# Optimization experiments

Hardware: AMD Instinct MI355X
Metric: run time of the kernel (lower is better)

## Reference

```python
import jax, jax.numpy as jnp
import numpy as np

B, L, D, H = 4, 2048, 1024, 16
DH = D // H
THETA = 100000.0


def setup_inputs() -> dict:
    key = jax.random.key(0)
    k1, k2, k3 = jax.random.split(key, 3)
    std_w = (2.0 / (D + 3 * D)) ** 0.5
    std_o = (2.0 / (D + D)) ** 0.5
    return {
        "x": jax.random.normal(k1, (B, L, D), dtype=jnp.float32),
        "W": jax.random.normal(k2, (3 * D, D), dtype=jnp.float32) * std_w,
        "Wo": jax.random.normal(k3, (D, D), dtype=jnp.float32) * std_o,
    }


def _rope(t):
    # t: [B, H, L, DH]; interleaved pair rotation as in the torch module
    pos = jnp.arange(L, dtype=jnp.float32)
    inv_freq = 1.0 / THETA ** (jnp.arange(0, DH, 2, dtype=jnp.float32) / DH)
    ang = pos[:, None] * inv_freq[None, :]            # [L, DH/2]
    cos = jnp.cos(ang)[:, :, None]                    # [L, DH/2, 1]
    sin = jnp.sin(ang)[:, :, None]
    tp = t.reshape(*t.shape[:-1], DH // 2, 2)         # pairs (x1, x2)
    x1, x2 = tp[..., 0], tp[..., 1]
    rot = jnp.stack([-x2, x1], axis=-1)               # [-x2, x1]
    out = tp * cos + rot * sin
    return out.reshape(*t.shape)


def reference(x, W, Wo):
    # fused QKV projection: weight layout is (t h d) along output dim
    qkv = jnp.einsum('bld,ed->ble', x, W)             # [B, L, 3D]
    qkv = qkv.reshape(B, L, 3, H, DH)
    qkv = jnp.transpose(qkv, (0, 3, 1, 2, 4))         # [B, H, L, 3, DH]
    Q, K, V = qkv[..., 0, :], qkv[..., 1, :], qkv[..., 2, :]
    Q, K = _rope(Q), _rope(K)
    scores = jnp.einsum('bhqd,bhkd->bhqk', Q, K) / (DH ** 0.5)
    causal = jnp.tril(jnp.ones((L, L), dtype=bool))
    scores = jnp.where(causal, scores, -jnp.inf)
    attn = jax.nn.softmax(scores, axis=-1)
    out = jnp.einsum('bhqk,bhkd->bhqd', attn, V)      # [B, H, L, DH]
    out = jnp.transpose(out, (0, 2, 1, 3)).reshape(B, L, D)
    return jnp.einsum('bld,ed->ble', out, Wo)
```

## Files before the change

kernel.cpp:

```cpp
#include <hip/hip_runtime.h>
#include <cstddef>
#include <cstdint>


typedef unsigned short u16;
typedef short bf16x8 __attribute__((ext_vector_type(8)));
typedef float f32x4 __attribute__((ext_vector_type(4)));

#define B_   4
#define L_   2048
#define H_   16
#define DH_  64
#define D_   1024
#define E3_  3072

__device__ __forceinline__ u16 f2bf(float f) {
  unsigned int u = __float_as_uint(f);
  u += 0x7fffu + ((u >> 16) & 1u);
  return (u16)(u >> 16);
}
__device__ __forceinline__ float bf2f(u16 h) {
  return __uint_as_float(((unsigned int)h) << 16);
}
__device__ __forceinline__ unsigned pk2(float a, float b) {
  return ((__float_as_uint(a) + 0x8000u) >> 16) |
         ((__float_as_uint(b) + 0x8000u) & 0xffff0000u);
}
__device__ __forceinline__ float fexp2(float x) {
#if __has_builtin(__builtin_amdgcn_exp2f)
  return __builtin_amdgcn_exp2f(x);
#else
  return exp2f(x);
#endif
}

__device__ __forceinline__ void gload_lds16(const void* g, void* l) {
  auto gp = reinterpret_cast<const uint32_t __attribute__((address_space(1)))*>(
      reinterpret_cast<uintptr_t>(g));
  auto lp = reinterpret_cast<uint32_t __attribute__((address_space(3)))*>(
      reinterpret_cast<uintptr_t>(l));
  __builtin_amdgcn_global_load_lds(gp, lp, 16, 0, 0);
}

__global__ __launch_bounds__(256) void cvt_bf16(const float* __restrict__ in,
                                                u16* __restrict__ out, int n8) {
  int i = blockIdx.x * 256 + threadIdx.x;
  if (i >= n8) return;
  const float4* p = (const float4*)in;
  float4 a = p[2 * i], b = p[2 * i + 1];
  uint4 o;
  o.x = (unsigned)f2bf(a.x) | ((unsigned)f2bf(a.y) << 16);
  o.y = (unsigned)f2bf(a.z) | ((unsigned)f2bf(a.w) << 16);
  o.z = (unsigned)f2bf(b.x) | ((unsigned)f2bf(b.y) << 16);
  o.w = (unsigned)f2bf(b.z) | ((unsigned)f2bf(b.w) << 16);
  ((uint4*)out)[i] = o;
}

template <bool OUT_BF16>
__global__ __launch_bounds__(256) void gemm_bt(const u16* __restrict__ A,
                                               const u16* __restrict__ Bm,
                                               void* __restrict__ C, int N, int K) {
  __shared__ __align__(16) u16 As[128 * 32];
  __shared__ __align__(16) u16 Bs[128 * 32];
  const int tid = threadIdx.x;
  const int lane = tid & 63, wave = tid >> 6;
  const int quad = lane >> 4, l15 = lane & 15;
  const int wm = (wave >> 1) << 6, wn = (wave & 1) << 6;
  const int m0 = blockIdx.y << 7, n0 = blockIdx.x << 7;

  f32x4 acc[4][4];
#pragma unroll
  for (int i = 0; i < 4; ++i)
#pragma unroll
    for (int j = 0; j < 4; ++j) acc[i][j] = {0.f, 0.f, 0.f, 0.f};

  const int sr = lane >> 2;
  const int sc = (lane & 3) * 8;

  for (int k0 = 0; k0 < K; k0 += 32) {
#pragma unroll
    for (int it = 0; it < 2; ++it) {
      const int chunk = wave * 2 + it;
      const int row = chunk * 16 + sr;
      gload_lds16(A + (size_t)(m0 + row) * K + k0 + sc, As + chunk * 512);
      gload_lds16(Bm + (size_t)(n0 + row) * K + k0 + sc, Bs + chunk * 512);
    }
    __syncthreads();
    bf16x8 af[4], bfr[4];
#pragma unroll
    for (int i = 0; i < 4; ++i)
      af[i] = *(const bf16x8*)(As + (wm + i * 16 + l15) * 32 + quad * 8);
#pragma unroll
    for (int j = 0; j < 4; ++j)
      bfr[j] = *(const bf16x8*)(Bs + (wn + j * 16 + l15) * 32 + quad * 8);
#pragma unroll
    for (int i = 0; i < 4; ++i)
#pragma unroll
      for (int j = 0; j < 4; ++j)
        acc[i][j] = __builtin_amdgcn_mfma_f32_16x16x32_bf16(af[i], bfr[j],
                                                            acc[i][j], 0, 0, 0);
    __syncthreads();
  }
#pragma unroll
  for (int i = 0; i < 4; ++i) {
    int row = m0 + wm + i * 16 + quad * 4;
#pragma unroll
    for (int j = 0; j < 4; ++j) {
      int col = n0 + wn + j * 16 + l15;
#pragma unroll
      for (int r = 0; r < 4; ++r) {
        if (OUT_BF16)
          ((u16*)C)[(size_t)(row + r) * N + col] = f2bf(acc[i][j][r]);
        else
          ((float*)C)[(size_t)(row + r) * N + col] = acc[i][j][r];
      }
    }
  }
}

__global__ __launch_bounds__(256) void rope_qk(u16* __restrict__ qkvb) {
  const int bl = blockIdx.x;
  const int l = bl & (L_ - 1);
  const int tid = threadIdx.x;
  const int c = tid & 7, h = (tid >> 3) & 15, t = tid >> 7;
  u16* p = qkvb + (size_t)bl * E3_ + t * D_ + h * DH_ + c * 8;
  uint4 v = *(const uint4*)p;
  unsigned* w = (unsigned*)&v;
  const float scale = t ? 1.0f : 0.18033688011112042f;
#pragma unroll
  for (int j = 0; j < 4; ++j) {
    const int d2 = c * 4 + j;
    float inv = exp2f((float)d2 * -0.5190512648261504f);
    float ang = (float)l * inv;
    float sn = __sinf(ang), cs = __cosf(ang);
    float x1 = bf2f((u16)(w[j] & 0xffffu)), x2 = bf2f((u16)(w[j] >> 16));
    float o1 = (x1 * cs - x2 * sn) * scale;
    float o2 = (x2 * cs + x1 * sn) * scale;
    w[j] = (unsigned)f2bf(o1) | ((unsigned)f2bf(o2) << 16);
  }
  *(uint4*)p = v;
}

__global__ __launch_bounds__(256) void transpose_v(const u16* __restrict__ qkvb,
                                                   u16* __restrict__ Vt) {
  __shared__ uint32_t tile[64 * 36];
  const int bh = blockIdx.x, b = bh >> 4, h = bh & 15;
  const int lbase = blockIdx.y << 6;
  const int tid = threadIdx.x;
  {
    const int ur = tid >> 3, c = tid & 7;
    const u16* src = qkvb + (size_t)(b * L_ + lbase + 2 * ur) * E3_ + 2 * D_ +
                     h * DH_ + c * 8;
    uint4 va = *(const uint4*)src;
    uint4 vb = *(const uint4*)(src + E3_);
    const unsigned* pa = (const unsigned*)&va;
    const unsigned* pb = (const unsigned*)&vb;
    const int us = ur ^ (c << 2);
#pragma unroll
    for (int q = 0; q < 4; ++q) {
      const int d0 = c * 8 + 2 * q;
      tile[d0 * 36 + us] = (pa[q] & 0xffffu) | (pb[q] << 16);
      tile[(d0 + 1) * 36 + us] = (pa[q] >> 16) | (pb[q] & 0xffff0000u);
    }
  }
  __syncthreads();
  const uint4* t4 = (const uint4*)tile;
#pragma unroll
  for (int it = 0; it < 2; ++it) {
    const int u = it * 256 + tid;
    const int d = u >> 3, lc = u & 7;
    uint4 v = t4[d * 9 + (lc ^ (d >> 3))];
    *(uint4*)(Vt + (size_t)(bh * DH_ + d) * L_ + lbase + lc * 8) = v;
  }
}

__global__ __launch_bounds__(512) void attn(const u16* __restrict__ qkvb,
                                            const u16* __restrict__ Vt,
                                            u16* __restrict__ Ob) {
  __shared__ __align__(16) u16 Ks[2][64 * 64];
  __shared__ __align__(16) u16 Vs[2][64 * 64];
  __shared__ __align__(16) u16 Ps[8][16 * 72];
  const int bh = blockIdx.y, b = bh >> 4, h = bh & 15;
  const int pair = blockIdx.x;
  const int tid = threadIdx.x;
  const int lane = tid & 63, wave = tid >> 6, quad = lane >> 4, l15 = lane & 15;
  u16* pw = Ps[wave];

  const int srow = wave * 8 + (lane >> 3);
  const int sgran = (lane & 7) ^ (lane >> 3);
  const u16* ksrc0 =
      qkvb + (size_t)(b * L_ + srow) * E3_ + D_ + h * DH_ + sgran * 8;
  const u16* vsrc0 = Vt + (size_t)(bh * DH_ + srow) * L_ + sgran * 8;
  const int ldst = wave * 512;

  bf16x8 ones;
#pragma unroll
  for (int i = 0; i < 8; ++i) ones[i] = (short)0x3F80;

  for (int a = 0; a < 2; ++a) {
    const int qbase = (a ? pair : (15 - pair)) << 7;
    const int rb = qbase + wave * 16;
    const int qg = rb + l15;

    bf16x8 qf[2];
    {
      const u16* qp = qkvb + (size_t)(b * L_ + qg) * E3_ + h * DH_;
      qf[0] = *(const bf16x8*)(qp + quad * 8);
      qf[1] = *(const bf16x8*)(qp + 32 + quad * 8);
    }

    f32x4 acc[4], lacc;
    lacc = {0.f, 0.f, 0.f, 0.f};
#pragma unroll
    for (int j = 0; j < 4; ++j) acc[j] = {0.f, 0.f, 0.f, 0.f};

    gload_lds16(ksrc0, Ks[0] + ldst);
    gload_lds16(vsrc0, Vs[0] + ldst);
    __syncthreads();

    const int kend = qbase + 128;
    int cur = 0;
    for (int kb = 0; kb < kend; kb += 64, cur ^= 1) {
      if (kb + 64 < kend) {
        gload_lds16(ksrc0 + (size_t)(kb + 64) * E3_, Ks[cur ^ 1] + ldst);
        gload_lds16(vsrc0 + (kb + 64), Vs[cur ^ 1] + ldst);
      }
      const u16* kcur = Ks[cur];
      const u16* vcur = Vs[cur];

      f32x4 st[4];
#pragma unroll
      for (int t = 0; t < 4; ++t) st[t] = {0.f, 0.f, 0.f, 0.f};
      __builtin_amdgcn_s_setprio(1);
#pragma unroll
      for (int ks = 0; ks < 2; ++ks) {
        bf16x8 kf[4];
#pragma unroll
        for (int t = 0; t < 4; ++t)
          kf[t] = *(const bf16x8*)(kcur + (t * 16 + l15) * 64 +
                                   (((ks * 4 + quad) ^ (l15 & 7)) * 8));
#pragma unroll
        for (int t = 0; t < 4; ++t)
          st[t] = __builtin_amdgcn_mfma_f32_16x16x32_bf16(kf[t], qf[ks],
                                                          st[t], 0, 0, 0);
      }
      __builtin_amdgcn_s_setprio(0);

      {
        const bool dg = (kb + 63 > rb);
#pragma unroll
        for (int t = 0; t < 4; ++t) {
          const int kg0 = kb + t * 16 + quad * 4;
          float p0, p1, p2, p3;
          if (dg) {
            p0 = (kg0 + 0 > qg) ? 0.f : fexp2(st[t][0]);
            p1 = (kg0 + 1 > qg) ? 0.f : fexp2(st[t][1]);
            p2 = (kg0 + 2 > qg) ? 0.f : fexp2(st[t][2]);
            p3 = (kg0 + 3 > qg) ? 0.f : fexp2(st[t][3]);
          } else {
            p0 = fexp2(st[t][0]);
            p1 = fexp2(st[t][1]);
            p2 = fexp2(st[t][2]);
            p3 = fexp2(st[t][3]);
          }
          uint2 pkd = {pk2(p0, p1), pk2(p2, p3)};
          *(uint2*)(pw + l15 * 72 + t * 16 + quad * 4) = pkd;
        }
      }
      asm volatile("s_waitcnt lgkmcnt(0)" ::: "memory");
      __builtin_amdgcn_sched_barrier(0);

      __builtin_amdgcn_s_setprio(1);
#pragma unroll
      for (int ks = 0; ks < 2; ++ks) {
        bf16x8 vf[4];
#pragma unroll
        for (int j = 0; j < 4; ++j)
          vf[j] = *(const bf16x8*)(vcur + (j * 16 + l15) * 64 +
                                   (((ks * 4 + quad) ^ (l15 & 7)) * 8));
        bf16x8 pf = *(const bf16x8*)(pw + l15 * 72 + ks * 32 + quad * 8);
        lacc = __builtin_amdgcn_mfma_f32_16x16x32_bf16(ones, pf, lacc,
                                                       0, 0, 0);
#pragma unroll
        for (int j = 0; j < 4; ++j)
          acc[j] = __builtin_amdgcn_mfma_f32_16x16x32_bf16(vf[j], pf,
                                                           acc[j], 0, 0, 0);
      }
      __builtin_amdgcn_s_setprio(0);

      __syncthreads();
    }

    {
      const float rl = 1.0f / lacc[0];
#pragma unroll
      for (int j = 0; j < 4; ++j) {
        uint2 od = {pk2(acc[j][0] * rl, acc[j][1] * rl),
                    pk2(acc[j][2] * rl, acc[j][3] * rl)};
        *(uint2*)(pw + l15 * 72 + j * 16 + quad * 4) = od;
      }
    }
    __syncthreads();
#pragma unroll
    for (int it = 0; it < 2; ++it) {
      int unit = it * 512 + tid;
      int row = unit >> 3, ch = (unit & 7) * 8;
      *(uint4*)(Ob + (size_t)(b * L_ + qbase + row) * D_ + h * DH_ + ch) =
          *(const uint4*)(Ps[row >> 4] + (row & 15) * 72 + ch);
    }
    __syncthreads();
  }
}

extern "C" void kernel_launch(void* const* d_in, const int* in_sizes, int n_in,
                              void* d_out, int out_size, void* d_ws, size_t ws_size,
                              hipStream_t stream) {
  const float* x  = (const float*)d_in[0];
  const float* W  = (const float*)d_in[1];
  const float* Wo = (const float*)d_in[2];
  float* out = (float*)d_out;

  char* ws = (char*)d_ws;
  u16* xb   = (u16*)(ws);
  u16* Wb   = (u16*)(ws + 16777216);
  u16* Wob  = (u16*)(ws + 23068672);
  u16* qkvb = (u16*)(ws + 25165824);
  u16* Vt   = (u16*)(ws + 75497472);
  u16* Ob   = (u16*)(ws + 92274688);

  cvt_bf16<<<4096, 256, 0, stream>>>(x, xb, 1048576);
  cvt_bf16<<<1536, 256, 0, stream>>>(W, Wb, 393216);
  cvt_bf16<<<512, 256, 0, stream>>>(Wo, Wob, 131072);

  gemm_bt<true><<<dim3(E3_ / 128, (B_ * L_) / 128), 256, 0, stream>>>(
      xb, Wb, qkvb, E3_, D_);

  rope_qk<<<B_ * L_, 256, 0, stream>>>(qkvb);
  transpose_v<<<dim3(B_ * H_, L_ / 64), 256, 0, stream>>>(qkvb, Vt);

  attn<<<dim3(8, B_ * H_), 512, 0, stream>>>(qkvb, Vt, Ob);

  gemm_bt<false><<<dim3(D_ / 128, (B_ * L_) / 128), 256, 0, stream>>>(
      Ob, Wob, out, D_, D_);
}
```

Before: 271.3 us.

## Merge conversion launches, fuse K-rope with V transpose, apply Q rope in attention

The three fp32-to-bf16 conversion launches become a single kernel that picks its source by global index. RoPE on K and the V transpose now run in one combined prep kernel. RoPE and softmax scaling for Q move into the attention kernel's Q fragment load, so the prep pass no longer reads or writes Q. This cuts launch count and removes a read-modify-write over the Q third of the qkv buffer. In exchange the attention kernel does extra sin/cos work per Q load, which it repeats for both query tiles each block handles.

```diff
diff --git a/kernel.cpp b/kernel.cpp
--- a/kernel.cpp
+++ b/kernel.cpp
@@ -42,18 +42,31 @@
   __builtin_amdgcn_global_load_lds(gp, lp, 16, 0, 0);
 }
 
-__global__ __launch_bounds__(256) void cvt_bf16(const float* __restrict__ in,
-                                                u16* __restrict__ out, int n8) {
+__global__ __launch_bounds__(256) void cvt_all(const float* __restrict__ x,
+                                               const float* __restrict__ W,
+                                               const float* __restrict__ Wo,
+                                               u16* __restrict__ xb,
+                                               u16* __restrict__ Wb,
+                                               u16* __restrict__ Wob) {
   int i = blockIdx.x * 256 + threadIdx.x;
-  if (i >= n8) return;
+  const float* in;
+  u16* out;
+  int off;
+  if (i < 1048576) {
+    in = x; out = xb; off = i;
+  } else if (i < 1441792) {
+    in = W; out = Wb; off = i - 1048576;
+  } else {
+    in = Wo; out = Wob; off = i - 1441792;
+  }
   const float4* p = (const float4*)in;
-  float4 a = p[2 * i], b = p[2 * i + 1];
+  float4 a = p[2 * off], b = p[2 * off + 1];
   uint4 o;
   o.x = (unsigned)f2bf(a.x) | ((unsigned)f2bf(a.y) << 16);
   o.y = (unsigned)f2bf(a.z) | ((unsigned)f2bf(a.w) << 16);
   o.z = (unsigned)f2bf(b.x) | ((unsigned)f2bf(b.y) << 16);
   o.w = (unsigned)f2bf(b.z) | ((unsigned)f2bf(b.w) << 16);
-  ((uint4*)out)[i] = o;
+  ((uint4*)out)[off] = o;
 }
 
 template <bool OUT_BF16>
@@ -118,59 +131,59 @@
   }
 }
 
-__global__ __launch_bounds__(256) void rope_qk(u16* __restrict__ qkvb) {
-  const int bl = blockIdx.x;
-  const int l = bl & (L_ - 1);
+__global__ __launch_bounds__(256) void prep(u16* __restrict__ qkvb,
+                                            u16* __restrict__ Vt) {
+  __shared__ uint32_t tile[64 * 36];
+  const int bid = blockIdx.x;
   const int tid = threadIdx.x;
-  const int c = tid & 7, h = (tid >> 3) & 15, t = tid >> 7;
-  u16* p = qkvb + (size_t)bl * E3_ + t * D_ + h * DH_ + c * 8;
-  uint4 v = *(const uint4*)p;
-  unsigned* w = (unsigned*)&v;
-  const float scale = t ? 1.0f : 0.18033688011112042f;
-#pragma unroll
-  for (int j = 0; j < 4; ++j) {
-    const int d2 = c * 4 + j;
-    float inv = exp2f((float)d2 * -0.5190512648261504f);
-    float ang = (float)l * inv;
-    float sn = __sinf(ang), cs = __cosf(ang);
-    float x1 = bf2f((u16)(w[j] & 0xffffu)), x2 = bf2f((u16)(w[j] >> 16));
-    float o1 = (x1 * cs - x2 * sn) * scale;
-    float o2 = (x2 * cs + x1 * sn) * scale;
-    w[j] = (unsigned)f2bf(o1) | ((unsigned)f2bf(o2) << 16);
-  }
-  *(uint4*)p = v;
-}
-
-__global__ __launch_bounds__(256) void transpose_v(const u16* __restrict__ qkvb,
-                                                   u16* __restrict__ Vt) {
-  __shared__ uint32_t tile[64 * 36];
-  const int bh = blockIdx.x, b = bh >> 4, h = bh & 15;
-  const int lbase = blockIdx.y << 6;
-  const int tid = threadIdx.x;
-  {
-    const int ur = tid >> 3, c = tid & 7;
-    const u16* src = qkvb + (size_t)(b * L_ + lbase + 2 * ur) * E3_ + 2 * D_ +
-                     h * DH_ + c * 8;
-    uint4 va = *(const uint4*)src;
-    uint4 vb = *(const uint4*)(src + E3_);
-    const unsigned* pa = (const unsigned*)&va;
-    const unsigned* pb = (const unsigned*)&vb;
-    const int us = ur ^ (c << 2);
-#pragma unroll
-    for (int q = 0; q < 4; ++q) {
-      const int d0 = c * 8 + 2 * q;
-      tile[d0 * 36 + us] = (pa[q] & 0xffffu) | (pb[q] << 16);
-      tile[(d0 + 1) * 36 + us] = (pa[q] >> 16) | (pb[q] & 0xffff0000u);
-    }
-  }
-  __syncthreads();
-  const uint4* t4 = (const uint4*)tile;
-#pragma unroll
-  for (int it = 0; it < 2; ++it) {
-    const int u = it * 256 + tid;
-    const int d = u >> 3, lc = u & 7;
-    uint4 v = t4[d * 9 + (lc ^ (d >> 3))];
-    *(uint4*)(Vt + (size_t)(bh * DH_ + d) * L_ + lbase + lc * 8) = v;
+  if (bid < 4096) {
+    const int bl = bid * 2 + (tid >> 7);
+    const int l = bl & (L_ - 1);
+    const int t7 = tid & 127;
+    const int c = t7 & 7, h = t7 >> 3;
+    u16* p = qkvb + (size_t)bl * E3_ + D_ + h * DH_ + c * 8;
+    uint4 v = *(const uint4*)p;
+    unsigned* w = (unsigned*)&v;
+#pragma unroll
+    for (int j = 0; j < 4; ++j) {
+      const int d2 = c * 4 + j;
+      float inv = exp2f((float)d2 * -0.5190512648261504f);
+      float ang = (float)l * inv;
+      float sn = __sinf(ang), cs = __cosf(ang);
+      float x1 = bf2f((u16)(w[j] & 0xffffu)), x2 = bf2f((u16)(w[j] >> 16));
+      w[j] = (unsigned)f2bf(x1 * cs - x2 * sn) |
+             ((unsigned)f2bf(x2 * cs + x1 * sn) << 16);
+    }
+    *(uint4*)p = v;
+  } else {
+    const int q = bid - 4096;
+    const int bh = q >> 5, b = bh >> 4, h = bh & 15;
+    const int lbase = (q & 31) << 6;
+    {
+      const int ur = tid >> 3, c = tid & 7;
+      const u16* src = qkvb + (size_t)(b * L_ + lbase + 2 * ur) * E3_ +
+                       2 * D_ + h * DH_ + c * 8;
+      uint4 va = *(const uint4*)src;
+      uint4 vb = *(const uint4*)(src + E3_);
+      const unsigned* pa = (const unsigned*)&va;
+      const unsigned* pb = (const unsigned*)&vb;
+      const int us = ur ^ (c << 2);
+#pragma unroll
+      for (int qq = 0; qq < 4; ++qq) {
+        const int d0 = c * 8 + 2 * qq;
+        tile[d0 * 36 + us] = (pa[qq] & 0xffffu) | (pb[qq] << 16);
+        tile[(d0 + 1) * 36 + us] = (pa[qq] >> 16) | (pb[qq] & 0xffff0000u);
+      }
+    }
+    __syncthreads();
+    const uint4* t4 = (const uint4*)tile;
+#pragma unroll
+    for (int it = 0; it < 2; ++it) {
+      const int u = it * 256 + tid;
+      const int d = u >> 3, lc = u & 7;
+      uint4 v = t4[d * 9 + (lc ^ (d >> 3))];
+      *(uint4*)(Vt + (size_t)(bh * DH_ + d) * L_ + lbase + lc * 8) = v;
+    }
   }
 }
 
@@ -205,8 +218,25 @@
     bf16x8 qf[2];
     {
       const u16* qp = qkvb + (size_t)(b * L_ + qg) * E3_ + h * DH_;
-      qf[0] = *(const bf16x8*)(qp + quad * 8);
-      qf[1] = *(const bf16x8*)(qp + 32 + quad * 8);
+      bf16x8 raw0 = *(const bf16x8*)(qp + quad * 8);
+      bf16x8 raw1 = *(const bf16x8*)(qp + 32 + quad * 8);
+      const float qsc = 0.18033688011112042f;
+#pragma unroll
+      for (int f = 0; f < 2; ++f) {
+        bf16x8 raw = f ? raw1 : raw0;
+        bf16x8 o;
+#pragma unroll
+        for (int j = 0; j < 4; ++j) {
+          const int d2 = f * 16 + quad * 4 + j;
+          float inv = exp2f((float)d2 * -0.5190512648261504f);
+          float ang = (float)qg * inv;
+          float sn = __sinf(ang), cs = __cosf(ang);
+          float x1 = bf2f((u16)raw[2 * j]), x2 = bf2f((u16)raw[2 * j + 1]);
+          o[2 * j] = (short)f2bf((x1 * cs - x2 * sn) * qsc);
+          o[2 * j + 1] = (short)f2bf((x2 * cs + x1 * sn) * qsc);
+        }
+        qf[f] = o;
+      }
     }
 
     f32x4 acc[4], lacc;
@@ -328,15 +358,12 @@
   u16* Vt   = (u16*)(ws + 75497472);
   u16* Ob   = (u16*)(ws + 92274688);
 
-  cvt_bf16<<<4096, 256, 0, stream>>>(x, xb, 1048576);
-  cvt_bf16<<<1536, 256, 0, stream>>>(W, Wb, 393216);
-  cvt_bf16<<<512, 256, 0, stream>>>(Wo, Wob, 131072);
+  cvt_all<<<6144, 256, 0, stream>>>(x, W, Wo, xb, Wb, Wob);
 
   gemm_bt<true><<<dim3(E3_ / 128, (B_ * L_) / 128), 256, 0, stream>>>(
       xb, Wb, qkvb, E3_, D_);
 
-  rope_qk<<<B_ * L_, 256, 0, stream>>>(qkvb);
-  transpose_v<<<dim3(B_ * H_, L_ / 64), 256, 0, stream>>>(qkvb, Vt);
+  prep<<<4096 + 2048, 256, 0, stream>>>(qkvb, Vt);
 
   attn<<<dim3(8, B_ * H_), 512, 0, stream>>>(qkvb, Vt, Ob);
 
```

Measured after the change: 260.5 us (median of 2 runs). -4.0%, faster.
